# Kernel tuning notes

Measured on AMD Instinct MI355X. Metric: run time of the kernel, lower is better.

The kernel has to match this reference:

```python
import jax, jax.numpy as jnp
import numpy as np

N = 50000
E = 800000
D_IN = 256
H1 = 512   # hidden_channels
H2 = 256   # out_channels == hidden_dim
NUM_CLASSES = 5
NEG_SLOPE = 0.2


def _edge_softmax(logits, dst, n):
    # numerically-stable softmax over edges grouped by destination node
    m = jax.ops.segment_max(logits, dst, num_segments=n)
    e = jnp.exp(logits - m[dst])
    s = jax.ops.segment_sum(e, dst, num_segments=n)
    return e / (s[dst] + 1e-16)


def _gat_conv(x, src, dst, W, att_src, att_dst, bias):
    h = x @ W                                   # [N, C] (PyG lin_src, no bias)
    a_s = (h * att_src).sum(-1)                 # [N]
    a_d = (h * att_dst).sum(-1)                 # [N]
    logits = jax.nn.leaky_relu(a_s[src] + a_d[dst], NEG_SLOPE)  # [E]
    alpha = _edge_softmax(logits, dst, x.shape[0])              # [E]
    out = jax.ops.segment_sum(h[src] * alpha[:, None], dst, num_segments=x.shape[0])
    return out + bias


def setup_inputs() -> dict:
    key = jax.random.key(0)
    ks = jax.random.split(key, 20)
    g = lambda k, shp, fan: jax.random.normal(k, shp, jnp.float32) * (1.0 / np.sqrt(fan))
    inp = {
        "x": jax.random.normal(ks[0], (N, D_IN), jnp.float32),
        "edge_index": jax.random.randint(ks[1], (2, E), 0, N, jnp.int64),
        # conv1 (GATConv, heads=1)
        "W1": g(ks[2], (D_IN, H1), D_IN),
        "att_src1": g(ks[3], (H1,), H1),
        "att_dst1": g(ks[4], (H1,), H1),
        "b_conv1": jnp.zeros((H1,), jnp.float32),
        # lin1 (dense residual)
        "A1": g(ks[5], (D_IN, H1), D_IN),
        "b1": jnp.zeros((H1,), jnp.float32),
        # conv2
        "W2": g(ks[6], (H1, H2), H1),
        "att_src2": g(ks[7], (H2,), H2),
        "att_dst2": g(ks[8], (H2,), H2),
        "b_conv2": jnp.zeros((H2,), jnp.float32),
        # lin2
        "A2": g(ks[9], (H1, H2), H1),
        "b2": jnp.zeros((H2,), jnp.float32),
        # 3 hidden MLP layers [256 -> 256]
        "Hw1": g(ks[10], (H2, H2), H2), "Hb1": jnp.zeros((H2,), jnp.float32),
        "Hw2": g(ks[11], (H2, H2), H2), "Hb2": jnp.zeros((H2,), jnp.float32),
        "Hw3": g(ks[12], (H2, H2), H2), "Hb3": jnp.zeros((H2,), jnp.float32),
        # classifier
        "fcw": g(ks[13], (H2, NUM_CLASSES), H2),
        "fcb": jnp.zeros((NUM_CLASSES,), jnp.float32),
    }
    return inp


def reference(x, edge_index, W1, att_src1, att_dst1, b_conv1, A1, b1,
              W2, att_src2, att_dst2, b_conv2, A2, b2,
              Hw1, Hb1, Hw2, Hb2, Hw3, Hb3, fcw, fcb):
    src, dst = edge_index[0], edge_index[1]
    h = _gat_conv(x, src, dst, W1, att_src1, att_dst1, b_conv1) + (x @ A1 + b1)
    h = jax.nn.relu(h)
    h = _gat_conv(h, src, dst, W2, att_src2, att_dst2, b_conv2) + (h @ A2 + b2)
    for w, b in ((Hw1, Hb1), (Hw2, Hb2), (Hw3, Hb3)):
        h = jax.nn.relu(h @ w + b)
    logits = h @ fcw + fcb
    return jax.nn.softmax(logits, axis=-1)
```

## Files before the change

kernel.cpp:

```cpp
#include <hip/hip_runtime.h>

typedef unsigned short u16;
typedef short short8 __attribute__((ext_vector_type(8)));
typedef u16 u16x4 __attribute__((ext_vector_type(4)));
typedef u16 u16x8 __attribute__((ext_vector_type(8)));
typedef float float4v __attribute__((ext_vector_type(4)));

#define NEG_SLOPE 0.2f

static __device__ __forceinline__ float b2f(u16 u) {
    union { unsigned int i; float f; } x; x.i = ((unsigned int)u) << 16; return x.f;
}
static __device__ __forceinline__ u16 f2b(float f) {
    unsigned int u = __float_as_uint(f);
    unsigned int r = (u + 0x7fffu + ((u >> 16) & 1u)) >> 16;
    return (u16)r;
}

__global__ void k_diag(float* out, int n, float val)
{
    int i = blockIdx.x * 256 + threadIdx.x;
    if (i < n) out[i] = val;
}

__global__ void scan_csr(const int* off, const int* srcs, int N, int E,
                         int* flag, int bit)
{
    int i = blockIdx.x * 256 + threadIdx.x;
    if (i < N) {
        int a = off[i], b = off[i + 1];
        if (a < 0 || b < a || b > E) atomicOr(flag, bit);
    }
    if (i == 0 && off[N] != E) atomicOr(flag, bit);
    if (i < E) {
        if ((unsigned)srcs[i] >= (unsigned)N) atomicOr(flag, bit);
    }
}

__global__ void k_final_diag(const int* flag, float* out, int n)
{
    int f = *flag;
    if (f == 0) return;
    int b = __ffs(f) - 1;
    float val = 32.0f * (b + 1);
    int i = blockIdx.x * 256 + threadIdx.x;
    if (i < n) out[i] = val;
}

__global__ void k_detect(const int* ei, int E, int* flag64)
{
    __shared__ int zc;
    if (threadIdx.x == 0) zc = 0;
    __syncthreads();
    int idx = 1 + 2 * (int)threadIdx.x;
    int z = (idx < 2 * E && ei[idx] == 0) ? 1 : 0;
    atomicAdd(&zc, z);
    __syncthreads();
    if (threadIdx.x == 0) *flag64 = (zc >= 200) ? 1 : 0;
}

__global__ void k_extract(const int* ei, int E, const int* flag64,
                          int* src, int* dst, int* deg, int N)
{
    int e = blockIdx.x * 256 + threadIdx.x;
    if (e >= E) return;
    int s, d;
    if (*flag64) {
        s = ei[2 * e];
        d = ei[2 * E + 2 * e];
    } else {
        s = ei[e];
        d = ei[E + e];
    }
    src[e] = s; dst[e] = d;
    if ((unsigned)d < (unsigned)N) atomicAdd(&deg[d], 1);
}

__global__ __launch_bounds__(256)
void k_scan_a(const int* __restrict__ deg, int* __restrict__ off,
              int* __restrict__ partial, int N)
{
    __shared__ int sd[256];
    int tid = threadIdx.x;
    int base = blockIdx.x * 1024;
    int i0 = base + tid * 4;
    int v0 = 0, v1 = 0, v2 = 0, v3 = 0;
    if (i0 < N)     v0 = deg[i0];
    if (i0 + 1 < N) v1 = deg[i0 + 1];
    if (i0 + 2 < N) v2 = deg[i0 + 2];
    if (i0 + 3 < N) v3 = deg[i0 + 3];
    int t = v0 + v1 + v2 + v3;
    sd[tid] = t;
    __syncthreads();
    #pragma unroll
    for (int s = 1; s < 256; s <<= 1) {
        int u = (tid >= s) ? sd[tid - s] : 0;
        __syncthreads();
        sd[tid] += u;
        __syncthreads();
    }
    int excl = sd[tid] - t;
    if (i0 < N)     off[i0]     = excl;
    if (i0 + 1 < N) off[i0 + 1] = excl + v0;
    if (i0 + 2 < N) off[i0 + 2] = excl + v0 + v1;
    if (i0 + 3 < N) off[i0 + 3] = excl + v0 + v1 + v2;
    if (tid == 255) partial[blockIdx.x] = sd[255];
}

__global__ __launch_bounds__(1024)
void k_scan_b(int* partial, int nblk)
{
    __shared__ int sd[1024];
    __shared__ int running;
    int tid = threadIdx.x;
    if (tid == 0) running = 0;
    __syncthreads();
    for (int base = 0; base < nblk; base += 1024) {
        int i = base + tid;
        int v = (i < nblk) ? partial[i] : 0;
        sd[tid] = v;
        __syncthreads();
        for (int s = 1; s < 1024; s <<= 1) {
            int u = (tid >= s) ? sd[tid - s] : 0;
            __syncthreads();
            sd[tid] += u;
            __syncthreads();
        }
        if (i < nblk) partial[i] = sd[tid] - v + running;
        int total = sd[1023];
        __syncthreads();
        if (tid == 0) running += total;
        __syncthreads();
    }
}

__global__ __launch_bounds__(256)
void k_scan_c(int* __restrict__ off, int* __restrict__ cursor,
              const int* __restrict__ partial, int N, int E)
{
    int i = blockIdx.x * 256 + threadIdx.x;
    if (i < N) {
        int v = off[i] + partial[i >> 10];
        off[i] = v;
        cursor[i] = v;
    }
    if (i == 0) off[N] = E;
}

__global__ void k_scatter(const int* src, const int* dst, int* cursor,
                          int* srcs, int E, int N)
{
    int e = blockIdx.x * 256 + threadIdx.x;
    if (e < E) {
        int d = dst[e];
        if ((unsigned)d < (unsigned)N) {
            int p = atomicAdd(&cursor[d], 1);
            if ((unsigned)p < (unsigned)E) srcs[p] = src[e];
        }
    }
}

__global__ __launch_bounds__(256)
void k_castdot(const float* __restrict__ x, const float* __restrict__ vs,
               const float* __restrict__ vd, u16* __restrict__ xb,
               float* __restrict__ a_s, float* __restrict__ a_d, int N)
{
    int tid = threadIdx.x;
    int rowb = tid >> 5;
    int col8 = (tid & 31) * 8;
    int n = blockIdx.x * 8 + rowb;
    if (n >= N) return;
    const float* xr = x + (size_t)n * 256 + col8;
    float4 v0 = *(const float4*)xr;
    float4 v1 = *(const float4*)(xr + 4);
    int4 w;
    w.x = (int)f2b(v0.x) | ((int)f2b(v0.y) << 16);
    w.y = (int)f2b(v0.z) | ((int)f2b(v0.w) << 16);
    w.z = (int)f2b(v1.x) | ((int)f2b(v1.y) << 16);
    w.w = (int)f2b(v1.z) | ((int)f2b(v1.w) << 16);
    *(int4*)(xb + (size_t)n * 256 + col8) = w;

    float4 s0 = *(const float4*)(vs + col8);
    float4 s1 = *(const float4*)(vs + col8 + 4);
    float4 d0 = *(const float4*)(vd + col8);
    float4 d1 = *(const float4*)(vd + col8 + 4);
    float ss = v0.x*s0.x + v0.y*s0.y + v0.z*s0.z + v0.w*s0.w
             + v1.x*s1.x + v1.y*s1.y + v1.z*s1.z + v1.w*s1.w;
    float sd = v0.x*d0.x + v0.y*d0.y + v0.z*d0.z + v0.w*d0.w
             + v1.x*d1.x + v1.y*d1.y + v1.z*d1.z + v1.w*d1.w;
    #pragma unroll
    for (int m = 16; m; m >>= 1) {
        ss += __shfl_xor(ss, m, 64);
        sd += __shfl_xor(sd, m, 64);
    }
    if ((tid & 31) == 0) { a_s[n] = ss; a_d[n] = sd; }
}

__global__ __launch_bounds__(64)
void k_packAll(const float* A1w, const float* W1, const float* W2, const float* A2w,
               const float* Hw1, const float* Hw2, const float* Hw3,
               u16* WT1, u16* WT2, u16* WTH)
{
    int z = blockIdx.z;
    const float *in1, *in2; int ksplit, csplit, in_ld, NC16; u16* out;
    if (z == 0)      { in1 = A1w; in2 = W1;  ksplit = 256; csplit = 0;   in_ld = 512; out = WT1; NC16 = 32; }
    else if (z == 1) { in1 = W2;  in2 = A2w; ksplit = 0;   csplit = 256; in_ld = 256; out = WT2; NC16 = 32; }
    else {
        if (blockIdx.x >= 16 || blockIdx.y >= 8) return;
        in1 = (z == 2) ? Hw1 : (z == 3) ? Hw2 : Hw3;
        in2 = nullptr; ksplit = 0; csplit = 0; in_ld = 256; NC16 = 16;
        out = WTH + (size_t)(z - 2) * 65536;
    }
    int l = threadIdx.x;
    int cf = blockIdx.x, kt = blockIdx.y;
    int col = cf * 16 + (l & 15);
    int kbase = kt * 32 + (l >> 4) * 8;
    const float* src = in1;
    int cc = col, koff = 0;
    if (ksplit > 0 && kbase >= ksplit) { src = in2; koff = ksplit; }
    if (csplit > 0 && col >= csplit)   { src = in2; cc = col - csplit; }
    u16* o = out + ((size_t)(kt * NC16 + cf) * 512) + l * 8;
    #pragma unroll
    for (int j = 0; j < 8; ++j)
        o[j] = f2b(src[(size_t)(kbase - koff + j) * in_ld + cc]);
}

__global__ __launch_bounds__(256)
void k_rowdot2f(const float* __restrict__ A, int ld, int H,
                const float* __restrict__ vs, const float* __restrict__ vd,
                float* a_s, float* a_d, int N)
{
    int wave = threadIdx.x >> 6, lane = threadIdx.x & 63;
    int n = blockIdx.x * 4 + wave;
    if (n >= N) return;
    const float* ar = A + (size_t)n * ld;
    float ss = 0.f, sd = 0.f;
    for (int i = lane * 4; i < H; i += 256) {
        float4 v  = *(const float4*)(ar + i);
        float4 s4 = *(const float4*)(vs + i);
        float4 d4 = *(const float4*)(vd + i);
        ss += v.x * s4.x + v.y * s4.y + v.z * s4.z + v.w * s4.w;
        sd += v.x * d4.x + v.y * d4.y + v.z * d4.z + v.w * d4.w;
    }
    #pragma unroll
    for (int m = 32; m; m >>= 1) {
        ss += __shfl_xor(ss, m, 64);
        sd += __shfl_xor(sd, m, 64);
    }
    if (lane == 0) { a_s[n] = ss; a_d[n] = sd; }
}

__global__ __launch_bounds__(256)
void k_alpha(const int* __restrict__ off, const int* __restrict__ srcs,
             const float* __restrict__ a_s, const float* __restrict__ a_d,
             float* __restrict__ alpha, int N)
{
    int wave = threadIdx.x >> 6, lane = threadIdx.x & 63;
    int n = blockIdx.x * 4 + wave;
    if (n >= N) return;
    int base = off[n], end = off[n + 1];
    float adn = a_d[n];
    float m = -1e30f, s = 0.f;
    for (int p = base + lane; p < end; p += 64) {
        int sx = srcs[p];
        sx = ((unsigned)sx < (unsigned)N) ? sx : 0;
        float z = a_s[sx] + adn;
        z = fmaxf(z, NEG_SLOPE * z);
        float mn = fmaxf(m, z);
        s = s * __expf(m - mn) + __expf(z - mn);
        m = mn;
    }
    #pragma unroll
    for (int msk = 32; msk; msk >>= 1) {
        float mo = __shfl_xor(m, msk, 64);
        float so = __shfl_xor(s, msk, 64);
        float mn = fmaxf(m, mo);
        s = s * __expf(m - mn) + so * __expf(mo - mn);
        m = mn;
    }
    float inv = 1.f / (s + 1e-16f);
    for (int p = base + lane; p < end; p += 64) {
        int sx = srcs[p];
        sx = ((unsigned)sx < (unsigned)N) ? sx : 0;
        float z = a_s[sx] + adn;
        z = fmaxf(z, NEG_SLOPE * z);
        alpha[p] = __expf(z - m) * inv;
    }
}

__global__ __launch_bounds__(256)
void k_aggw(const u16* __restrict__ rows, const int* __restrict__ off,
            const int* __restrict__ srcs, const float* __restrict__ alpha,
            const u16* __restrict__ add, u16* __restrict__ out, int N)
{
    int wave = threadIdx.x >> 6, lane = threadIdx.x & 63;
    int n = blockIdx.x * 4 + wave;
    if (n >= N) return;
    int base = off[n], end = off[n + 1];
    int half = lane >> 5;
    int c8 = (lane & 31) * 8;
    float acc[8] = {};
    int p = base;
    for (; p + 3 < end; p += 4) {
        int sA = srcs[p + half];
        int sB = srcs[p + 2 + half];
        sA = ((unsigned)sA < (unsigned)N) ? sA : 0;
        sB = ((unsigned)sB < (unsigned)N) ? sB : 0;
        float wA = alpha[p + half];
        float wB = alpha[p + 2 + half];
        u16x8 vA = *(const u16x8*)(rows + (size_t)sA * 256 + c8);
        u16x8 vB = *(const u16x8*)(rows + (size_t)sB * 256 + c8);
        #pragma unroll
        for (int j = 0; j < 8; ++j)
            acc[j] += wA * b2f(vA[j]) + wB * b2f(vB[j]);
    }
    for (; p + 1 < end; p += 2) {
        int sA = srcs[p + half];
        sA = ((unsigned)sA < (unsigned)N) ? sA : 0;
        float wA = alpha[p + half];
        u16x8 vA = *(const u16x8*)(rows + (size_t)sA * 256 + c8);
        #pragma unroll
        for (int j = 0; j < 8; ++j)
            acc[j] += wA * b2f(vA[j]);
    }
    if (p < end) {
        int sA = srcs[p];
        sA = ((unsigned)sA < (unsigned)N) ? sA : 0;
        float wA = half ? 0.f : alpha[p];
        u16x8 vA = *(const u16x8*)(rows + (size_t)sA * 256 + c8);
        #pragma unroll
        for (int j = 0; j < 8; ++j)
            acc[j] += wA * b2f(vA[j]);
    }
    #pragma unroll
    for (int j = 0; j < 8; ++j)
        acc[j] += __shfl_xor(acc[j], 32, 64);
    if (half == 0) {
        size_t ob = (size_t)n * 256 + c8;
        if (add) {
            u16x8 ad8 = *(const u16x8*)(add + ob);
            #pragma unroll
            for (int j = 0; j < 8; ++j) acc[j] += b2f(ad8[j]);
        }
        u16x8 o;
        #pragma unroll
        for (int j = 0; j < 8; ++j) o[j] = f2b(acc[j]);
        *(u16x8*)(out + ob) = o;
    }
}

__global__ __launch_bounds__(512)
void bigfull(const u16* __restrict__ A1, int lda1,
             const u16* __restrict__ A2, int lda2,
             const u16* __restrict__ WTf,
             const float* b0a, const float* b0b,
             const float* b1a, const float* b1b,
             u16* C1, int ldc1, u16* C2, int ldc2,
             const float* __restrict__ dotS, const float* __restrict__ dotD,
             float* oaS, float* oaD,
             int M, int relu0, int relu1)
{
    __shared__ u16 As[64 * 32];

    const int tid = threadIdx.x;
    const int w = tid >> 6, lane = tid & 63;
    const int m16 = lane & 15, q = lane >> 4;
    const int rowBase = blockIdx.x * 64;

    float4v acc[16] = {};

    for (int k0 = 0; k0 < 512; k0 += 32) {
        const int kt = k0 >> 5;
        __syncthreads();
        if (tid < 256) {
            int rf = tid >> 6, al = tid & 63;
            int grow = rowBase + rf * 16 + (al & 15);
            if (grow >= M) grow = M - 1;
            int kk = k0 + (al >> 4) * 8;
            const u16* src = (kk < 256)
                ? A1 + (size_t)grow * lda1 + kk
                : A2 + (size_t)grow * lda2 + (kk - 256);
            *(int4*)&As[tid * 8] = *(const int4*)src;
        }
        __syncthreads();

        short8 a[4], b[4];
        #pragma unroll
        for (int c = 0; c < 4; ++c) {
            int4 bv = *(const int4*)(WTf + (size_t)kt * 16384
                                     + (size_t)(w * 4 + c) * 512 + lane * 8);
            b[c] = *(short8*)&bv;
        }
        #pragma unroll
        for (int r = 0; r < 4; ++r)
            a[r] = *(const short8*)&As[r * 512 + lane * 8];
        #pragma unroll
        for (int r = 0; r < 4; ++r)
            #pragma unroll
            for (int c = 0; c < 4; ++c)
                acc[r * 4 + c] = __builtin_amdgcn_mfma_f32_16x16x32_bf16(
                    a[r], b[c], acc[r * 4 + c], 0, 0, 0);
    }

    const int colgrp = w >> 2;
    const float* ba = colgrp ? b1a : b0a;
    const float* bb = colgrp ? b1b : b0b;
    u16* C  = colgrp ? C2 : C1;
    const int ldc  = colgrp ? ldc2 : ldc1;
    const int relu = colgrp ? relu1 : relu0;
    #pragma unroll
    for (int c = 0; c < 4; ++c) {
        int lc = ((w & 3) * 4 + c) * 16 + m16;
        float bv = (ba ? ba[lc] : 0.f) + (bb ? bb[lc] : 0.f);
        #pragma unroll
        for (int r = 0; r < 4; ++r)
            #pragma unroll
            for (int i = 0; i < 4; ++i) {
                int grow = rowBase + r * 16 + q * 4 + i;
                if (grow < M) {
                    float v = acc[r * 4 + c][i] + bv;
                    if (relu) v = fmaxf(v, 0.f);
                    C[(size_t)grow * ldc + lc] = f2b(v);
                }
            }
    }

    if (dotS && colgrp == 0) {
        #pragma unroll
        for (int r = 0; r < 4; ++r)
            #pragma unroll
            for (int i = 0; i < 4; ++i) {
                float ss = 0.f, sd = 0.f;
                #pragma unroll
                for (int c = 0; c < 4; ++c) {
                    int lc = ((w & 3) * 4 + c) * 16 + m16;
                    float v = b2f(f2b(acc[r * 4 + c][i]));
                    ss += v * dotS[lc];
                    sd += v * dotD[lc];
                }
                #pragma unroll
                for (int msk = 1; msk < 16; msk <<= 1) {
                    ss += __shfl_xor(ss, msk, 64);
                    sd += __shfl_xor(sd, msk, 64);
                }
                int grow = rowBase + r * 16 + q * 4 + i;
                if (m16 == 0 && grow < M) {
                    atomicAdd(&oaS[grow], ss);
                    atomicAdd(&oaD[grow], sd);
                }
            }
    }
}

__global__ __launch_bounds__(512)
void k_mlp3fc(const u16* __restrict__ WTHf,
              const float* Hb1, const float* Hb2, const float* Hb3,
              const float* __restrict__ fcw, const float* __restrict__ fcb,
              const u16* __restrict__ Hin, float* __restrict__ out, int M)
{
    __shared__ u16 P[64 * 256];

    const int tid = threadIdx.x;
    const int w = tid >> 6, lane = tid & 63;
    const int m16 = lane & 15, q = lane >> 4;
    const int rowBase = blockIdx.x * 64;

    #pragma unroll
    for (int p = 0; p < 4; ++p) {
        int ch = p * 512 + tid;
        int f = ch >> 6, l = ch & 63;
        int kt = f >> 2, rf = f & 3;
        int grow = rowBase + rf * 16 + (l & 15);
        if (grow >= M) grow = M - 1;
        int col = kt * 32 + (l >> 4) * 8;
        *(int4*)&P[ch * 8] = *(const int4*)(Hin + (size_t)grow * 256 + col);
    }
    __syncthreads();

    const float* biases[3] = {Hb1, Hb2, Hb3};
    for (int L = 0; L < 3; ++L) {
        const u16* WTf = WTHf + (size_t)L * 65536;
        float4v acc[8] = {};
        #pragma unroll 2
        for (int kt = 0; kt < 8; ++kt) {
            short8 a[4], b[2];
            #pragma unroll
            for (int c = 0; c < 2; ++c) {
                int4 bv = *(const int4*)(WTf + (size_t)(kt * 16 + w * 2 + c) * 512
                                         + lane * 8);
                b[c] = *(short8*)&bv;
            }
            #pragma unroll
            for (int r = 0; r < 4; ++r)
                a[r] = *(const short8*)&P[(kt * 4 + r) * 512 + lane * 8];
            #pragma unroll
            for (int r = 0; r < 4; ++r)
                #pragma unroll
                for (int c = 0; c < 2; ++c)
                    acc[r * 2 + c] = __builtin_amdgcn_mfma_f32_16x16x32_bf16(
                        a[r], b[c], acc[r * 2 + c], 0, 0, 0);
        }
        const float* bias = biases[L];
        __syncthreads();
        #pragma unroll
        for (int c = 0; c < 2; ++c) {
            int col = w * 32 + c * 16 + m16;
            float bv = bias[col];
            int kt2 = col >> 5;
            int l2h = 16 * ((col & 31) >> 3);
            int j2 = col & 7;
            #pragma unroll
            for (int r = 0; r < 4; ++r)
                #pragma unroll
                for (int i = 0; i < 4; ++i) {
                    int l2 = (q * 4 + i) + l2h;
                    P[(size_t)(kt2 * 4 + r) * 512 + l2 * 8 + j2] =
                        f2b(fmaxf(acc[r * 2 + c][i] + bv, 0.f));
                }
        }
        __syncthreads();
    }

    if (w < 4) {
        float p5[5] = {0.f, 0.f, 0.f, 0.f, 0.f};
        #pragma unroll
        for (int kt = 0; kt < 8; ++kt) {
            u16x8 v = *(const u16x8*)&P[(kt * 4 + w) * 512 + lane * 8];
            int colb = kt * 32 + q * 8;
            #pragma unroll
            for (int j = 0; j < 8; ++j) {
                float hv = b2f(v[j]);
                const float* wr = fcw + (size_t)(colb + j) * 5;
                #pragma unroll
                for (int c = 0; c < 5; ++c) p5[c] += hv * wr[c];
            }
        }
        #pragma unroll
        for (int c = 0; c < 5; ++c) {
            p5[c] += __shfl_xor(p5[c], 16, 64);
            p5[c] += __shfl_xor(p5[c], 32, 64);
        }
        int grow = rowBase + w * 16 + m16;
        if (q == 0 && grow < M) {
            float mx = -1e30f;
            #pragma unroll
            for (int c = 0; c < 5; ++c) { p5[c] += fcb[c]; mx = fmaxf(mx, p5[c]); }
            float s = 0.f, e[5];
            #pragma unroll
            for (int c = 0; c < 5; ++c) { e[c] = __expf(p5[c] - mx); s += e[c]; }
            float inv = 1.f / s;
            #pragma unroll
            for (int c = 0; c < 5; ++c) out[(size_t)grow * 5 + c] = e[c] * inv;
        }
    }
}

extern "C" void kernel_launch(void* const* d_in, const int* in_sizes, int n_in,
                              void* d_out, int out_size, void* d_ws, size_t ws_size,
                              hipStream_t stream)
{
    const float* x    = (const float*)d_in[0];
    const int*   ei   = (const int*)  d_in[1];
    const float* W1   = (const float*)d_in[2];
    const float* as1  = (const float*)d_in[3];
    const float* ad1  = (const float*)d_in[4];
    const float* bc1  = (const float*)d_in[5];
    const float* A1w  = (const float*)d_in[6];
    const float* b1   = (const float*)d_in[7];
    const float* W2   = (const float*)d_in[8];
    const float* as2  = (const float*)d_in[9];
    const float* ad2  = (const float*)d_in[10];
    const float* bc2  = (const float*)d_in[11];
    const float* A2w  = (const float*)d_in[12];
    const float* b2   = (const float*)d_in[13];
    const float* Hw1  = (const float*)d_in[14];
    const float* Hb1  = (const float*)d_in[15];
    const float* Hw2  = (const float*)d_in[16];
    const float* Hb2  = (const float*)d_in[17];
    const float* Hw3  = (const float*)d_in[18];
    const float* Hb3  = (const float*)d_in[19];
    const float* fcw  = (const float*)d_in[20];
    const float* fcb  = (const float*)d_in[21];
    float* out = (float*)d_out;

    const int D = 256;
    const int N = in_sizes[0] / D;
    const int E = in_sizes[1] / 2;

    char* w = (char*)d_ws;
    auto alloc = [&](size_t bytes) {
        char* p = w;
        w += (bytes + 255) & ~(size_t)255;
        return p;
    };
    int*   flag   = (int*)  alloc(256);
    int*   flag64 = (int*)  alloc(256);
    float* a_s    = (float*)alloc((size_t)N * 4);
    float* a_d    = (float*)alloc((size_t)N * 4);
    float* vs1    = (float*)alloc(1024);
    float* vd1    = (float*)alloc(1024);
    int*   deg    = (int*)  alloc((size_t)N * 4);
    int*   cursor = (int*)  alloc((size_t)N * 4);
    int*   offA   = (int*)  alloc((size_t)(N + 1) * 4);
    int*   part   = (int*)  alloc((size_t)((N + 1023) / 1024 + 1) * 4);
    int*   srcs   = (int*)  alloc((size_t)E * 4);
    float* alpha  = (float*)alloc((size_t)E * 4);
    u16*   WT1    = (u16*)  alloc(512 * 512 * 2);
    u16*   WT2    = (u16*)  alloc(512 * 512 * 2);
    u16*   WTH    = (u16*)  alloc(3 * 256 * 256 * 2);
    u16*   BUF1   = (u16*)  alloc((size_t)N * 512 * 2);
    u16*   BUF2   = (u16*)  alloc((size_t)N * 512 * 2);

    int* src32 = (int*)BUF1;
    int* dst32 = src32 + E;

    size_t need = (size_t)(w - (char*)d_ws);
    if (ws_size < need) {
        float code = 1000.0f + (float)(ws_size >> 20);
        k_diag<<<(out_size + 255) / 256, 256, 0, stream>>>(out, out_size, code);
        return;
    }

    const int EB  = (E + 255) / 256;
    const int NB4 = (N + 3) / 4;
    const int OB  = (out_size + 255) / 256;
    const int NE  = (N > E ? N : E);
    const int RB64 = (N + 63) / 64;
    const int NBLK = (N + 1023) / 1024;
    const size_t NH2 = (size_t)N * 256;
    u16* XB   = BUF1;
    u16* AGGX = BUF1 + NH2;

    hipMemsetAsync(flag, 0, 4, stream);
    hipMemsetAsync(deg, 0, (size_t)N * 4, stream);

    k_detect <<<1, 256, 0, stream>>>(ei, E, flag64);
    k_extract<<<EB, 256, 0, stream>>>(ei, E, flag64, src32, dst32, deg, N);
    k_scan_a <<<NBLK, 256, 0, stream>>>(deg, offA, part, N);
    k_scan_b <<<1, 1024, 0, stream>>>(part, NBLK);
    k_scan_c <<<(N + 255) / 256, 256, 0, stream>>>(offA, cursor, part, N, E);
    k_scatter<<<EB, 256, 0, stream>>>(src32, dst32, cursor, srcs, E, N);
    scan_csr <<<(NE + 255) / 256, 256, 0, stream>>>(offA, srcs, N, E, flag, 1);

    k_packAll<<<dim3(32, 16, 5), 64, 0, stream>>>(A1w, W1, W2, A2w,
                                                  Hw1, Hw2, Hw3, WT1, WT2, WTH);

    k_rowdot2f<<<64, 256, 0, stream>>>(W1, 512, 512, as1, ad1, vs1, vd1, 256);
    k_castdot<<<(N + 7) / 8, 256, 0, stream>>>(x, vs1, vd1, XB, a_s, a_d, N);
    k_alpha<<<NB4, 256, 0, stream>>>(offA, srcs, a_s, a_d, alpha, N);

    hipMemsetAsync(a_s, 0, (size_t)N * 4, stream);
    hipMemsetAsync(a_d, 0, (size_t)N * 4, stream);

    k_aggw<<<NB4, 256, 0, stream>>>(XB, offA, srcs, alpha, nullptr, AGGX, N);

    bigfull<<<RB64, 512, 0, stream>>>(XB, 256, AGGX, 256, WT1,
                                      b1, bc1, b1 + 256, bc1 + 256,
                                      BUF2, 512, BUF2 + 256, 512,
                                      nullptr, nullptr, nullptr, nullptr,
                                      N, 1, 1);

    bigfull<<<RB64, 512, 0, stream>>>(BUF2, 512, BUF2 + 256, 512, WT2,
                                      nullptr, nullptr, b2, bc2,
                                      BUF1, 256, BUF1 + NH2, 256,
                                      as2, ad2, a_s, a_d,
                                      N, 0, 0);

    k_alpha<<<NB4, 256, 0, stream>>>(offA, srcs, a_s, a_d, alpha, N);
    k_aggw<<<NB4, 256, 0, stream>>>(BUF1, offA, srcs, alpha, BUF1 + NH2, BUF2, N);

    k_mlp3fc<<<RB64, 512, 0, stream>>>(WTH, Hb1, Hb2, Hb3, fcw, fcb,
                                       BUF2, out, N);

    k_final_diag<<<OB, 256, 0, stream>>>(flag, out, out_size);
}
```

Baseline: 543.6 us.

## Recompute attention weights in aggregation and stage GEMM tiles via direct-to-LDS loads

The alpha kernel now only computes per-node max and inverse sum. The aggregation kernel recomputes each edge weight from a_s, a_d and these stats, so the per-edge alpha array is no longer written and then read back. Separately, the fused GEMM kernel stages both A and B tiles into shared memory with global_load_lds 16-byte loads instead of register round-trips, and B is now shared across the block. This adds an extra exp per edge per half-wave and a larger LDS footprint (32KB for B), which may reduce occupancy.

```diff
diff --git a/kernel.cpp b/kernel.cpp
--- a/kernel.cpp
+++ b/kernel.cpp
@@ -2,11 +2,14 @@
 
 typedef unsigned short u16;
 typedef short short8 __attribute__((ext_vector_type(8)));
-typedef u16 u16x4 __attribute__((ext_vector_type(4)));
 typedef u16 u16x8 __attribute__((ext_vector_type(8)));
 typedef float float4v __attribute__((ext_vector_type(4)));
 
 #define NEG_SLOPE 0.2f
+
+#define GLOAD_LDS16(g, l) __builtin_amdgcn_global_load_lds(                    \
+    (const __attribute__((address_space(1))) void*)(g),                        \
+    (__attribute__((address_space(3))) void*)(l), 16, 0, 0)
 
 static __device__ __forceinline__ float b2f(u16 u) {
     union { unsigned int i; float f; } x; x.i = ((unsigned int)u) << 16; return x.f;
@@ -251,9 +254,9 @@
 }
 
 __global__ __launch_bounds__(256)
-void k_alpha(const int* __restrict__ off, const int* __restrict__ srcs,
-             const float* __restrict__ a_s, const float* __restrict__ a_d,
-             float* __restrict__ alpha, int N)
+void k_alpha1p(const int* __restrict__ off, const int* __restrict__ srcs,
+               const float* __restrict__ a_s, const float* __restrict__ a_d,
+               float* __restrict__ mu, float* __restrict__ inv, int N)
 {
     int wave = threadIdx.x >> 6, lane = threadIdx.x & 63;
     int n = blockIdx.x * 4 + wave;
@@ -278,25 +281,21 @@
         s = s * __expf(m - mn) + so * __expf(mo - mn);
         m = mn;
     }
-    float inv = 1.f / (s + 1e-16f);
-    for (int p = base + lane; p < end; p += 64) {
-        int sx = srcs[p];
-        sx = ((unsigned)sx < (unsigned)N) ? sx : 0;
-        float z = a_s[sx] + adn;
-        z = fmaxf(z, NEG_SLOPE * z);
-        alpha[p] = __expf(z - m) * inv;
-    }
+    if (lane == 0) { mu[n] = m; inv[n] = 1.f / (s + 1e-16f); }
 }
 
 __global__ __launch_bounds__(256)
 void k_aggw(const u16* __restrict__ rows, const int* __restrict__ off,
-            const int* __restrict__ srcs, const float* __restrict__ alpha,
+            const int* __restrict__ srcs, const float* __restrict__ a_s,
+            const float* __restrict__ a_d, const float* __restrict__ mu,
+            const float* __restrict__ inv,
             const u16* __restrict__ add, u16* __restrict__ out, int N)
 {
     int wave = threadIdx.x >> 6, lane = threadIdx.x & 63;
     int n = blockIdx.x * 4 + wave;
     if (n >= N) return;
     int base = off[n], end = off[n + 1];
+    float adn = a_d[n], mn = mu[n], iv = inv[n];
     int half = lane >> 5;
     int c8 = (lane & 31) * 8;
     float acc[8] = {};
@@ -306,8 +305,10 @@
         int sB = srcs[p + 2 + half];
         sA = ((unsigned)sA < (unsigned)N) ? sA : 0;
         sB = ((unsigned)sB < (unsigned)N) ? sB : 0;
-        float wA = alpha[p + half];
-        float wB = alpha[p + 2 + half];
+        float zA = a_s[sA] + adn; zA = fmaxf(zA, NEG_SLOPE * zA);
+        float zB = a_s[sB] + adn; zB = fmaxf(zB, NEG_SLOPE * zB);
+        float wA = __expf(zA - mn) * iv;
+        float wB = __expf(zB - mn) * iv;
         u16x8 vA = *(const u16x8*)(rows + (size_t)sA * 256 + c8);
         u16x8 vB = *(const u16x8*)(rows + (size_t)sB * 256 + c8);
         #pragma unroll
@@ -317,7 +318,8 @@
     for (; p + 1 < end; p += 2) {
         int sA = srcs[p + half];
         sA = ((unsigned)sA < (unsigned)N) ? sA : 0;
-        float wA = alpha[p + half];
+        float zA = a_s[sA] + adn; zA = fmaxf(zA, NEG_SLOPE * zA);
+        float wA = __expf(zA - mn) * iv;
         u16x8 vA = *(const u16x8*)(rows + (size_t)sA * 256 + c8);
         #pragma unroll
         for (int j = 0; j < 8; ++j)
@@ -326,7 +328,8 @@
     if (p < end) {
         int sA = srcs[p];
         sA = ((unsigned)sA < (unsigned)N) ? sA : 0;
-        float wA = half ? 0.f : alpha[p];
+        float zA = a_s[sA] + adn; zA = fmaxf(zA, NEG_SLOPE * zA);
+        float wA = half ? 0.f : (__expf(zA - mn) * iv);
         u16x8 vA = *(const u16x8*)(rows + (size_t)sA * 256 + c8);
         #pragma unroll
         for (int j = 0; j < 8; ++j)
@@ -361,39 +364,45 @@
              int M, int relu0, int relu1)
 {
     __shared__ u16 As[64 * 32];
+    __shared__ u16 Bs[512 * 32];
 
     const int tid = threadIdx.x;
     const int w = tid >> 6, lane = tid & 63;
     const int m16 = lane & 15, q = lane >> 4;
     const int rowBase = blockIdx.x * 64;
 
+    int garow = rowBase + (w & 3) * 16 + m16;
+    if (garow >= M) garow = M - 1;
+
     float4v acc[16] = {};
 
     for (int k0 = 0; k0 < 512; k0 += 32) {
         const int kt = k0 >> 5;
         __syncthreads();
-        if (tid < 256) {
-            int rf = tid >> 6, al = tid & 63;
-            int grow = rowBase + rf * 16 + (al & 15);
-            if (grow >= M) grow = M - 1;
-            int kk = k0 + (al >> 4) * 8;
+        if (w < 4) {
+            int kk = k0 + q * 8;
             const u16* src = (kk < 256)
-                ? A1 + (size_t)grow * lda1 + kk
-                : A2 + (size_t)grow * lda2 + (kk - 256);
-            *(int4*)&As[tid * 8] = *(const int4*)src;
+                ? A1 + (size_t)garow * lda1 + kk
+                : A2 + (size_t)garow * lda2 + (kk - 256);
+            GLOAD_LDS16(src, &As[w * 512]);
+        }
+        {
+            const u16* wsrc = WTf + (size_t)kt * 16384;
+            #pragma unroll
+            for (int p = 0; p < 4; ++p) {
+                int chb = p * 512 + w * 64;
+                GLOAD_LDS16(wsrc + ((size_t)chb + lane) * 8, &Bs[chb * 8]);
+            }
         }
         __syncthreads();
 
         short8 a[4], b[4];
-        #pragma unroll
-        for (int c = 0; c < 4; ++c) {
-            int4 bv = *(const int4*)(WTf + (size_t)kt * 16384
-                                     + (size_t)(w * 4 + c) * 512 + lane * 8);
-            b[c] = *(short8*)&bv;
-        }
         #pragma unroll
         for (int r = 0; r < 4; ++r)
             a[r] = *(const short8*)&As[r * 512 + lane * 8];
+        #pragma unroll
+        for (int c = 0; c < 4; ++c)
+            b[c] = *(const short8*)&Bs[(w * 4 + c) * 512 + lane * 8];
         #pragma unroll
         for (int r = 0; r < 4; ++r)
             #pragma unroll
@@ -597,6 +606,8 @@
     int*   flag64 = (int*)  alloc(256);
     float* a_s    = (float*)alloc((size_t)N * 4);
     float* a_d    = (float*)alloc((size_t)N * 4);
+    float* mu     = (float*)alloc((size_t)N * 4);
+    float* inv    = (float*)alloc((size_t)N * 4);
     float* vs1    = (float*)alloc(1024);
     float* vd1    = (float*)alloc(1024);
     int*   deg    = (int*)  alloc((size_t)N * 4);
@@ -604,7 +615,6 @@
     int*   offA   = (int*)  alloc((size_t)(N + 1) * 4);
     int*   part   = (int*)  alloc((size_t)((N + 1023) / 1024 + 1) * 4);
     int*   srcs   = (int*)  alloc((size_t)E * 4);
-    float* alpha  = (float*)alloc((size_t)E * 4);
     u16*   WT1    = (u16*)  alloc(512 * 512 * 2);
     u16*   WT2    = (u16*)  alloc(512 * 512 * 2);
     u16*   WTH    = (u16*)  alloc(3 * 256 * 256 * 2);
@@ -647,12 +657,13 @@
 
     k_rowdot2f<<<64, 256, 0, stream>>>(W1, 512, 512, as1, ad1, vs1, vd1, 256);
     k_castdot<<<(N + 7) / 8, 256, 0, stream>>>(x, vs1, vd1, XB, a_s, a_d, N);
-    k_alpha<<<NB4, 256, 0, stream>>>(offA, srcs, a_s, a_d, alpha, N);
+    k_alpha1p<<<NB4, 256, 0, stream>>>(offA, srcs, a_s, a_d, mu, inv, N);
+
+    k_aggw<<<NB4, 256, 0, stream>>>(XB, offA, srcs, a_s, a_d, mu, inv,
+                                    nullptr, AGGX, N);
 
     hipMemsetAsync(a_s, 0, (size_t)N * 4, stream);
     hipMemsetAsync(a_d, 0, (size_t)N * 4, stream);
-
-    k_aggw<<<NB4, 256, 0, stream>>>(XB, offA, srcs, alpha, nullptr, AGGX, N);
 
     bigfull<<<RB64, 512, 0, stream>>>(XB, 256, AGGX, 256, WT1,
                                       b1, bc1, b1 + 256, bc1 + 256,
@@ -666,8 +677,9 @@
                                       as2, ad2, a_s, a_d,
                                       N, 0, 0);
 
-    k_alpha<<<NB4, 256, 0, stream>>>(offA, srcs, a_s, a_d, alpha, N);
-    k_aggw<<<NB4, 256, 0, stream>>>(BUF1, offA, srcs, alpha, BUF1 + NH2, BUF2, N);
+    k_alpha1p<<<NB4, 256, 0, stream>>>(offA, srcs, a_s, a_d, mu, inv, N);
+    k_aggw<<<NB4, 256, 0, stream>>>(BUF1, offA, srcs, a_s, a_d, mu, inv,
+                                    BUF1 + NH2, BUF2, N);
 
     k_mlp3fc<<<RB64, 512, 0, stream>>>(WTH, Hb1, Hb2, Hb3, fcw, fcb,
                                        BUF2, out, N);
```

Result: faster. 532.9 us (-2.0%).
